# Performance work log

Measured on AMD Instinct MI355X. Metric: run time of the kernel, lower is better.

The kernel has to match this reference:

```python
import jax, jax.numpy as jnp
import numpy as np

DIM = 256
K = 255
PAD = K // 2  # 127, 'same' padding


def _dwconv(x, w, b, pad_h, pad_w):
    # x: [N, C, H, W]; w: [C, 1, kh, kw] (OIHW with feature_group_count=C)
    y = jax.lax.conv_general_dilated(
        x, w,
        window_strides=(1, 1),
        padding=((pad_h, pad_h), (pad_w, pad_w)),
        dimension_numbers=("NCHW", "OIHW", "NCHW"),
        feature_group_count=x.shape[1],
    )
    return y + b[None, :, None, None]


def setup_inputs() -> dict:
    key = jax.random.key(0)
    k1, k2, k3, k4, k5 = jax.random.split(key, 5)
    x = jax.random.normal(k1, (10, DIM, 128, 128), dtype=jnp.float32)
    # depthwise weights, scaled like torch's kaiming-uniform fan_in=K
    scale = 1.0 / np.sqrt(K)
    wh = jax.random.uniform(k2, (DIM, 1, K, 1), jnp.float32, -scale, scale)
    bh = jax.random.uniform(k3, (DIM,), jnp.float32, -scale, scale)
    ww = jax.random.uniform(k4, (DIM, 1, 1, K), jnp.float32, -scale, scale)
    bw = jax.random.uniform(k5, (DIM,), jnp.float32, -scale, scale)
    return {"x": x, "wh": wh, "bh": bh, "ww": ww, "bw": bw}


def reference(x, wh, bh, ww, bw):
    # conv_h: (K,1) depthwise conv, padding (K//2, 0)
    x = _dwconv(x, wh, bh, PAD, 0)
    # conv_w: (1,K) depthwise conv, padding (0, K//2)
    x = _dwconv(x, ww, bw, 0, PAD)
    return x
```

## Files before the change

kernel.cpp:

```cpp
#include <hip/hip_runtime.h>

#define HW 128
#define KTAPS 255
#define DIMC 256

typedef short short8  __attribute__((ext_vector_type(8)));
typedef short short4v __attribute__((ext_vector_type(4)));
typedef float f32x16  __attribute__((ext_vector_type(16)));
typedef float f32x4   __attribute__((ext_vector_type(4)));

__device__ __forceinline__ short f2bf(float f) {
    return __builtin_bit_cast(short, (__bf16)f);
}
__device__ __forceinline__ int pad16(int c) { return c + (c >> 3); }

__device__ __forceinline__ void bar_lds() {
    asm volatile("s_waitcnt lgkmcnt(0)" ::: "memory");
    __builtin_amdgcn_s_barrier();
}


__global__ __launch_bounds__(1024, 4)
void sep_conv255_mfma(const float* __restrict__ x,
                      const float* __restrict__ wh,
                      const float* __restrict__ bh,
                      const float* __restrict__ ww,
                      const float* __restrict__ bw,
                      float* __restrict__ out,
                      int nslices) {
    __shared__ __align__(16) short PxA[2304 * 8];
    __shared__ __align__(16) short Py [2304 * 8];
    __shared__ __align__(16) short WB [1792 * 8];
    __shared__ __align__(16) float Zt [64 * 132];
    __shared__ float cw[HW];

    const int c    = blockIdx.x;
    const int tid  = threadIdx.x;
    const int lane = tid & 63;
    const int wv   = tid >> 6;
    const int wm   = wv >> 2;
    const int wn   = wv & 3;
    const int s31  = lane & 31;
    const int hi   = lane >> 5;

    const float* __restrict__ whc = wh + c * KTAPS;
    const float* __restrict__ wwc = ww + c * KTAPS;

    const int tw  = tid & 31;
    const int bh0 = tid >> 5;
    int stChunk[4];
#pragma unroll
    for (int i = 0; i < 4; ++i)
        stChunk[i] = ((i << 3) + (tw >> 2)) * 64 + bh0 + (((tw >> 1) & 1) << 5);
    const int stOff = (tw & 1) << 2;
    const size_t ldOff = (size_t)bh0 * HW + (tw << 2);

    f32x4 xv[4];
    {
        const float* xs = x + (size_t)c * (HW * HW);
#pragma unroll
        for (int i = 0; i < 4; ++i)
            xv[i] = *reinterpret_cast<const f32x4*>(&xs[ldOff + (size_t)(i << 5) * HW]);
    }
#pragma unroll
    for (int i = 0; i < 2; ++i) {
        const int ch = tid + (i << 10);
        if (ch < 1792) {
            const int isB = (ch >= 896);
            const int lc  = ch & 63;
            const int t   = (ch >> 6) - (isB ? 14 : 0);
            const float* ws = isB ? wwc : whc;
            const float* wp = ws + (31 + (t << 4) + ((lc >> 5) << 3) - (lc & 31));
            short8 v;
#pragma unroll
            for (int j = 0; j < 8; ++j) v[j] = f2bf(wp[j]);
            *reinterpret_cast<short8*>(&WB[ch * 8]) = v;
        }
    }
    if (tid < HW) {
        float s = 0.0f;
        for (int i = 0; i < HW; ++i) s += wwc[127 - tid + i];
        cw[tid] = bh[c] * s + bw[c];
    }
#pragma unroll
    for (int i = 0; i < 4; ++i) {
        short4v v;
#pragma unroll
        for (int j = 0; j < 4; ++j) v[j] = f2bf(xv[i][j]);
        *reinterpret_cast<short4v*>(&PxA[pad16(stChunk[i]) * 8 + stOff]) = v;
    }
    if (1 < nslices) {
        const float* xs = x + ((size_t)DIMC + c) * (HW * HW);
#pragma unroll
        for (int i = 0; i < 4; ++i)
            xv[i] = *reinterpret_cast<const f32x4*>(&xs[ldOff + (size_t)(i << 5) * HW]);
    }
    bar_lds();

    const int   kk     = (wn << 5) + s31;
    const float cwv    = cw[kk];
    const int   hbase  = (wm << 5) + (hi << 2);
    const int   rpBase = ((wn << 3) + (wm << 1)) * 64 + s31;

    for (int s = 0; s < nslices; ++s) {
        f32x16 acc;
#pragma unroll
        for (int j = 0; j < 16; ++j) acc[j] = 0.0f;
#pragma unroll
        for (int ks = 0; ks < 8; ++ks) {
            const short8 a = *reinterpret_cast<const short8*>(
                &PxA[pad16(((wm << 3) + ks) * 64 + lane) * 8]);
            const short8 b = *reinterpret_cast<const short8*>(
                &WB[(((ks - (wn << 1) + 20) << 6) + lane) * 8]);
            acc = __builtin_amdgcn_mfma_f32_32x32x16_bf16(a, b, acc, 0, 0, 0);
        }
#pragma unroll
        for (int r = 0; r < 16; ++r) {
            const int chunk = rpBase + ((r >> 3) << 6) + (((r >> 2) & 1) << 5);
            const int j     = (hi << 2) + (r & 3);
            Py[pad16(chunk) * 8 + j] = f2bf(acc[r]);
        }
        bar_lds();

        if (s + 1 < nslices) {
#pragma unroll
            for (int i = 0; i < 4; ++i) {
                short4v v;
#pragma unroll
                for (int j = 0; j < 4; ++j) v[j] = f2bf(xv[i][j]);
                *reinterpret_cast<short4v*>(&PxA[pad16(stChunk[i]) * 8 + stOff]) = v;
            }
        }
        if (s + 2 < nslices) {
            const float* xs = x + ((size_t)(s + 2) * DIMC + c) * (HW * HW);
#pragma unroll
            for (int i = 0; i < 4; ++i)
                xv[i] = *reinterpret_cast<const f32x4*>(&xs[ldOff + (size_t)(i << 5) * HW]);
        }

#pragma unroll
        for (int j = 0; j < 16; ++j) acc[j] = 0.0f;
#pragma unroll
        for (int ks = 0; ks < 8; ++ks) {
            const short8 a = *reinterpret_cast<const short8*>(
                &WB[(((ks - (wm << 1) + 6) << 6) + lane) * 8]);
            const short8 b = *reinterpret_cast<const short8*>(
                &Py[pad16(((wn << 3) + ks) * 64 + lane) * 8]);
            acc = __builtin_amdgcn_mfma_f32_32x32x16_bf16(a, b, acc, 0, 0, 0);
        }

        float* zc = out + ((size_t)s * DIMC + c) * (HW * HW);

        if (wm < 2) {
#pragma unroll
            for (int r = 0; r < 16; ++r) {
                const int h = hbase + (r & 3) + ((r >> 2) << 3);
                Zt[h * 132 + kk] = acc[r] + cwv;
            }
        }
        bar_lds();
#pragma unroll
        for (int i = 0; i < 2; ++i) {
            const int hh = bh0 + (i << 5);
            const f32x4 v = *reinterpret_cast<const f32x4*>(&Zt[hh * 132 + (tw << 2)]);
            *reinterpret_cast<f32x4*>(&zc[(size_t)hh * HW + (tw << 2)]) = v;
        }
        bar_lds();
        if (wm >= 2) {
#pragma unroll
            for (int r = 0; r < 16; ++r) {
                const int h = hbase + (r & 3) + ((r >> 2) << 3);
                Zt[(h - 64) * 132 + kk] = acc[r] + cwv;
            }
        }
        bar_lds();
#pragma unroll
        for (int i = 0; i < 2; ++i) {
            const int hh = bh0 + (i << 5);
            const f32x4 v = *reinterpret_cast<const f32x4*>(&Zt[hh * 132 + (tw << 2)]);
            *reinterpret_cast<f32x4*>(&zc[(size_t)(64 + hh) * HW + (tw << 2)]) = v;
        }
    }
}

extern "C" void kernel_launch(void* const* d_in, const int* in_sizes, int n_in,
                              void* d_out, int out_size, void* d_ws, size_t ws_size,
                              hipStream_t stream) {
    const float* x  = (const float*)d_in[0];
    const float* wh = (const float*)d_in[1];
    const float* bh = (const float*)d_in[2];
    const float* ww = (const float*)d_in[3];
    const float* bw = (const float*)d_in[4];
    float* outp = (float*)d_out;

    const int nbatch = in_sizes[0] / (DIMC * HW * HW);
    dim3 grid(DIMC);
    dim3 block(1024);
    hipLaunchKernelGGL(sep_conv255_mfma, grid, block, 0, stream,
                       x, wh, bh, ww, bw, outp, nbatch);
}
```

Baseline: 291.1 us.

## Split batch across two half-size blocks per channel and drop LDS weight/transpose staging

The grid doubles to two blocks per channel, each handling half the batch slices with 512 threads, and each wave now computes two 32x32 output tiles. The Toeplitz weight fragments are built straight from global memory on every use instead of being staged in an LDS table. Output goes straight from the accumulators to global memory, replacing the LDS transpose buffer and its extra barriers. The aim is more blocks in flight and less LDS traffic and synchronisation. The cost is uncoalesced scalar output stores and repeated global weight loads with bf16 conversion inside the MFMA loops.

```diff
diff --git a/kernel.cpp b/kernel.cpp
--- a/kernel.cpp
+++ b/kernel.cpp
@@ -19,8 +19,17 @@
     __builtin_amdgcn_s_barrier();
 }
 
+__device__ __forceinline__ short8 wfrag(const float* __restrict__ p) {
+    float t[8];
+    __builtin_memcpy(t, p, 32);
+    short8 v;
+#pragma unroll
+    for (int j = 0; j < 8; ++j) v[j] = f2bf(t[j]);
+    return v;
+}
 
-__global__ __launch_bounds__(1024, 4)
+
+__global__ __launch_bounds__(512, 4)
 void sep_conv255_mfma(const float* __restrict__ x,
                       const float* __restrict__ wh,
                       const float* __restrict__ bh,
@@ -30,156 +39,145 @@
                       int nslices) {
     __shared__ __align__(16) short PxA[2304 * 8];
     __shared__ __align__(16) short Py [2304 * 8];
-    __shared__ __align__(16) short WB [1792 * 8];
-    __shared__ __align__(16) float Zt [64 * 132];
     __shared__ float cw[HW];
 
-    const int c    = blockIdx.x;
+    const int c    = blockIdx.x >> 1;
+    const int half = blockIdx.x & 1;
     const int tid  = threadIdx.x;
     const int lane = tid & 63;
     const int wv   = tid >> 6;
-    const int wm   = wv >> 2;
-    const int wn   = wv & 3;
+    const int wm   = wv >> 1;
+    const int wn0  = wv & 1;
     const int s31  = lane & 31;
     const int hi   = lane >> 5;
+
+    const int ns2  = (nslices + 1) >> 1;
+    const int sbeg = half * ns2;
+    const int cnt  = min(ns2, nslices - sbeg);
+    if (cnt <= 0) return;
 
     const float* __restrict__ whc = wh + c * KTAPS;
     const float* __restrict__ wwc = ww + c * KTAPS;
 
-    const int tw  = tid & 31;
-    const int bh0 = tid >> 5;
-    int stChunk[4];
+    const int tw = tid & 31;
+    const int g  = tid >> 5;
+    const size_t ldOff = (size_t)g * HW + (tw << 2);
+    int stChunk[8];
 #pragma unroll
-    for (int i = 0; i < 4; ++i)
-        stChunk[i] = ((i << 3) + (tw >> 2)) * 64 + bh0 + (((tw >> 1) & 1) << 5);
+    for (int i = 0; i < 8; ++i) {
+        const int r = g + (i << 4);
+        stChunk[i] = (((r >> 5) << 3) + (tw >> 2)) * 64 + (r & 31) + (((tw >> 1) & 1) << 5);
+    }
     const int stOff = (tw & 1) << 2;
-    const size_t ldOff = (size_t)bh0 * HW + (tw << 2);
 
-    f32x4 xv[4];
+    f32x4 xv[8];
     {
-        const float* xs = x + (size_t)c * (HW * HW);
+        const float* xs = x + ((size_t)sbeg * DIMC + c) * (HW * HW);
 #pragma unroll
-        for (int i = 0; i < 4; ++i)
-            xv[i] = *reinterpret_cast<const f32x4*>(&xs[ldOff + (size_t)(i << 5) * HW]);
+        for (int i = 0; i < 8; ++i)
+            xv[i] = *reinterpret_cast<const f32x4*>(&xs[ldOff + (size_t)(i << 4) * HW]);
+    }
+    if (tid < HW) {
+        float ssum = 0.0f;
+        for (int i = 0; i < HW; ++i) ssum += wwc[127 - tid + i];
+        cw[tid] = bh[c] * ssum + bw[c];
     }
 #pragma unroll
-    for (int i = 0; i < 2; ++i) {
-        const int ch = tid + (i << 10);
-        if (ch < 1792) {
-            const int isB = (ch >= 896);
-            const int lc  = ch & 63;
-            const int t   = (ch >> 6) - (isB ? 14 : 0);
-            const float* ws = isB ? wwc : whc;
-            const float* wp = ws + (31 + (t << 4) + ((lc >> 5) << 3) - (lc & 31));
-            short8 v;
-#pragma unroll
-            for (int j = 0; j < 8; ++j) v[j] = f2bf(wp[j]);
-            *reinterpret_cast<short8*>(&WB[ch * 8]) = v;
-        }
-    }
-    if (tid < HW) {
-        float s = 0.0f;
-        for (int i = 0; i < HW; ++i) s += wwc[127 - tid + i];
-        cw[tid] = bh[c] * s + bw[c];
-    }
-#pragma unroll
-    for (int i = 0; i < 4; ++i) {
+    for (int i = 0; i < 8; ++i) {
         short4v v;
 #pragma unroll
         for (int j = 0; j < 4; ++j) v[j] = f2bf(xv[i][j]);
         *reinterpret_cast<short4v*>(&PxA[pad16(stChunk[i]) * 8 + stOff]) = v;
     }
-    if (1 < nslices) {
-        const float* xs = x + ((size_t)DIMC + c) * (HW * HW);
+    if (cnt > 1) {
+        const float* xs = x + ((size_t)(sbeg + 1) * DIMC + c) * (HW * HW);
 #pragma unroll
-        for (int i = 0; i < 4; ++i)
-            xv[i] = *reinterpret_cast<const f32x4*>(&xs[ldOff + (size_t)(i << 5) * HW]);
+        for (int i = 0; i < 8; ++i)
+            xv[i] = *reinterpret_cast<const f32x4*>(&xs[ldOff + (size_t)(i << 4) * HW]);
     }
     bar_lds();
 
-    const int   kk     = (wn << 5) + s31;
-    const float cwv    = cw[kk];
-    const int   hbase  = (wm << 5) + (hi << 2);
-    const int   rpBase = ((wn << 3) + (wm << 1)) * 64 + s31;
+    const float cwv0 = cw[(wn0 << 5) + s31];
+    const float cwv1 = cw[((wn0 + 2) << 5) + s31];
 
-    for (int s = 0; s < nslices; ++s) {
-        f32x16 acc;
+    const float* pb0 = wwc + (127 + (hi << 3) - s31 - (wn0 << 5));
+    const float* pa0 = whc + (127 + (hi << 3) - s31 - (wm  << 5));
+
+    for (int s = 0; s < cnt; ++s) {
+        f32x16 acc0, acc1;
 #pragma unroll
-        for (int j = 0; j < 16; ++j) acc[j] = 0.0f;
+        for (int j = 0; j < 16; ++j) { acc0[j] = 0.0f; acc1[j] = 0.0f; }
 #pragma unroll
         for (int ks = 0; ks < 8; ++ks) {
             const short8 a = *reinterpret_cast<const short8*>(
                 &PxA[pad16(((wm << 3) + ks) * 64 + lane) * 8]);
-            const short8 b = *reinterpret_cast<const short8*>(
-                &WB[(((ks - (wn << 1) + 20) << 6) + lane) * 8]);
-            acc = __builtin_amdgcn_mfma_f32_32x32x16_bf16(a, b, acc, 0, 0, 0);
+            const short8 b0 = wfrag(pb0 + (ks << 4));
+            const short8 b1 = wfrag(pb0 + (ks << 4) - 64);
+            acc0 = __builtin_amdgcn_mfma_f32_32x32x16_bf16(a, b0, acc0, 0, 0, 0);
+            acc1 = __builtin_amdgcn_mfma_f32_32x32x16_bf16(a, b1, acc1, 0, 0, 0);
         }
+
+        {
 #pragma unroll
-        for (int r = 0; r < 16; ++r) {
-            const int chunk = rpBase + ((r >> 3) << 6) + (((r >> 2) & 1) << 5);
-            const int j     = (hi << 2) + (r & 3);
-            Py[pad16(chunk) * 8 + j] = f2bf(acc[r]);
+            for (int q = 0; q < 4; ++q) {
+                const int chunk0 = ((wn0 << 3) + (wm << 1) + (q >> 1)) * 64 + s31 + ((q & 1) << 5);
+                short4v v;
+#pragma unroll
+                for (int j = 0; j < 4; ++j) v[j] = f2bf(acc0[(q << 2) + j]);
+                *reinterpret_cast<short4v*>(&Py[pad16(chunk0) * 8 + (hi << 2)]) = v;
+            }
+#pragma unroll
+            for (int q = 0; q < 4; ++q) {
+                const int chunk1 = (((wn0 + 2) << 3) + (wm << 1) + (q >> 1)) * 64 + s31 + ((q & 1) << 5);
+                short4v v;
+#pragma unroll
+                for (int j = 0; j < 4; ++j) v[j] = f2bf(acc1[(q << 2) + j]);
+                *reinterpret_cast<short4v*>(&Py[pad16(chunk1) * 8 + (hi << 2)]) = v;
+            }
         }
         bar_lds();
 
-        if (s + 1 < nslices) {
+        if (s + 1 < cnt) {
 #pragma unroll
-            for (int i = 0; i < 4; ++i) {
+            for (int i = 0; i < 8; ++i) {
                 short4v v;
 #pragma unroll
                 for (int j = 0; j < 4; ++j) v[j] = f2bf(xv[i][j]);
                 *reinterpret_cast<short4v*>(&PxA[pad16(stChunk[i]) * 8 + stOff]) = v;
             }
         }
-        if (s + 2 < nslices) {
-            const float* xs = x + ((size_t)(s + 2) * DIMC + c) * (HW * HW);
+        if (s + 2 < cnt) {
+            const float* xs = x + ((size_t)(sbeg + s + 2) * DIMC + c) * (HW * HW);
 #pragma unroll
-            for (int i = 0; i < 4; ++i)
-                xv[i] = *reinterpret_cast<const f32x4*>(&xs[ldOff + (size_t)(i << 5) * HW]);
+            for (int i = 0; i < 8; ++i)
+                xv[i] = *reinterpret_cast<const f32x4*>(&xs[ldOff + (size_t)(i << 4) * HW]);
         }
 
 #pragma unroll
-        for (int j = 0; j < 16; ++j) acc[j] = 0.0f;
+        for (int j = 0; j < 16; ++j) { acc0[j] = 0.0f; acc1[j] = 0.0f; }
 #pragma unroll
         for (int ks = 0; ks < 8; ++ks) {
-            const short8 a = *reinterpret_cast<const short8*>(
-                &WB[(((ks - (wm << 1) + 6) << 6) + lane) * 8]);
-            const short8 b = *reinterpret_cast<const short8*>(
-                &Py[pad16(((wn << 3) + ks) * 64 + lane) * 8]);
-            acc = __builtin_amdgcn_mfma_f32_32x32x16_bf16(a, b, acc, 0, 0, 0);
+            const short8 aw = wfrag(pa0 + (ks << 4));
+            const short8 B0 = *reinterpret_cast<const short8*>(
+                &Py[pad16(((wn0 << 3) + ks) * 64 + lane) * 8]);
+            const short8 B1 = *reinterpret_cast<const short8*>(
+                &Py[pad16((((wn0 + 2) << 3) + ks) * 64 + lane) * 8]);
+            acc0 = __builtin_amdgcn_mfma_f32_32x32x16_bf16(aw, B0, acc0, 0, 0, 0);
+            acc1 = __builtin_amdgcn_mfma_f32_32x32x16_bf16(aw, B1, acc1, 0, 0, 0);
         }
 
-        float* zc = out + ((size_t)s * DIMC + c) * (HW * HW);
-
-        if (wm < 2) {
+        {
+            float* zc = out + ((size_t)(sbeg + s) * DIMC + c) * (HW * HW);
+            const int w0 = (wn0 << 5) + s31;
+            const int hb = (wm << 5) + (hi << 2);
 #pragma unroll
             for (int r = 0; r < 16; ++r) {
-                const int h = hbase + (r & 3) + ((r >> 2) << 3);
-                Zt[h * 132 + kk] = acc[r] + cwv;
+                const int h = hb + (r & 3) + ((r >> 2) << 3);
+                zc[(size_t)h * HW + w0]      = acc0[r] + cwv0;
+                zc[(size_t)h * HW + w0 + 64] = acc1[r] + cwv1;
             }
         }
         bar_lds();
-#pragma unroll
-        for (int i = 0; i < 2; ++i) {
-            const int hh = bh0 + (i << 5);
-            const f32x4 v = *reinterpret_cast<const f32x4*>(&Zt[hh * 132 + (tw << 2)]);
-            *reinterpret_cast<f32x4*>(&zc[(size_t)hh * HW + (tw << 2)]) = v;
-        }
-        bar_lds();
-        if (wm >= 2) {
-#pragma unroll
-            for (int r = 0; r < 16; ++r) {
-                const int h = hbase + (r & 3) + ((r >> 2) << 3);
-                Zt[(h - 64) * 132 + kk] = acc[r] + cwv;
-            }
-        }
-        bar_lds();
-#pragma unroll
-        for (int i = 0; i < 2; ++i) {
-            const int hh = bh0 + (i << 5);
-            const f32x4 v = *reinterpret_cast<const f32x4*>(&Zt[hh * 132 + (tw << 2)]);
-            *reinterpret_cast<f32x4*>(&zc[(size_t)(64 + hh) * HW + (tw << 2)]) = v;
-        }
     }
 }
 
@@ -194,8 +192,8 @@
     float* outp = (float*)d_out;
 
     const int nbatch = in_sizes[0] / (DIMC * HW * HW);
-    dim3 grid(DIMC);
-    dim3 block(1024);
+    dim3 grid(DIMC * 2);
+    dim3 block(512);
     hipLaunchKernelGGL(sep_conv255_mfma, grid, block, 0, stream,
                        x, wh, bh, ww, bw, outp, nbatch);
 }
```

New measurement: 348.3 us. 1.2x slower.
